# Kernel optimization log

Measured on AMD Instinct MI355X. Metric: run time of the kernel, lower is better.

## Reference

```python
import jax, jax.numpy as jnp
import numpy as np

K_NEIGHBORS = 3  # init kwarg k_neighbors


def setup_inputs() -> dict:
    key = jax.random.key(0)
    k1, k2 = jax.random.split(key)
    q = jax.random.normal(k1, (75, 640, 21, 21), dtype=jnp.float32)
    S = jax.random.normal(k2, (5, 640, 21, 21), dtype=jnp.float32)
    return {"q": q, "S": S, "qAV_num": 1, "SAV_num": 1, "shot_num": 1}


def reference(q, S, qAV_num, SAV_num, shot_num):
    B, C = q.shape[0], q.shape[1]
    # [B, HW, C], L2-normalize each local descriptor over channels
    qd = q.reshape(B, C, -1).transpose(0, 2, 1)
    qd = qd / jnp.linalg.norm(qd, axis=2, keepdims=True)

    N = S.shape[0]
    sd = S.reshape(N, C, -1).transpose(0, 2, 1)  # [N, HW, C]
    sd = sd / jnp.linalg.norm(sd, axis=2, keepdims=True)
    HW = sd.shape[1]
    M = SAV_num * shot_num * HW
    # group support images into classes: [ncls, C, M]
    sup = sd.reshape(-1, M, C).transpose(0, 2, 1)
    ncls = sup.shape[0]

    # cosine similarity: [B, ncls, HW, M]
    ip = jnp.einsum('bqc,ncm->bnqm', qd, sup)
    # split AV groups: [B//qAV, qAV, ncls, HW, M]
    ip = ip.reshape(B // qAV_num, qAV_num, ncls, HW, M)
    # top-k along the query-descriptor (HW) axis (torch dim=-2)
    topk = jax.lax.top_k(jnp.swapaxes(ip, -1, -2), K_NEIGHBORS)[0]  # [..., M, k]
    img2class = topk.sum(axis=(-1, -2))  # [B', qAV, ncls]
    # geometric mean over the AV axis (dim=1)
    sim = jnp.exp(jnp.mean(jnp.log(img2class), axis=1))  # [B', ncls]
    return sim
```

## Files before the change

### kernel.cpp

```cpp
#include <hip/hip_runtime.h>
#include <hip/hip_bf16.h>


#define B_IMGS 75
#define N_CLS  5
#define C_DIM  640
#define HW     441
#define HWP    448
#define NKT    20
#define NRB    28
#define CHUNK  512

typedef __attribute__((ext_vector_type(8))) short  short8;
typedef __attribute__((ext_vector_type(4))) float  float4v;

__device__ __forceinline__ void ins3(float& t0, float& t1, float& t2, float v) {
    float m  = fminf(t0, v);
    t0 = fmaxf(t0, v);
    float m2 = fminf(t1, m);
    t1 = fmaxf(t1, m);
    t2 = fmaxf(t2, m2);
}

__device__ __forceinline__ void glds16(const __hip_bfloat16* g, __hip_bfloat16* l) {
    __builtin_amdgcn_global_load_lds(
        (const __attribute__((address_space(1))) unsigned int*)g,
        (__attribute__((address_space(3))) unsigned int*)l, 16, 0, 0);
}

__global__ __launch_bounds__(256)
void prep_kernel(const float* __restrict__ q, const float* __restrict__ S,
                 __hip_bfloat16* __restrict__ qn2, __hip_bfloat16* __restrict__ sn2) {
    __shared__ __hip_bfloat16 tile[C_DIM][65];
    __shared__ float part[4][64];
    __shared__ float inv[64];

    int bid = blockIdx.x;
    int img = bid / 7;
    int h0  = bid % 7;
    const float* src; __hip_bfloat16* dst;
    if (img < B_IMGS) {
        src = q + (size_t)img * C_DIM * HW;
        dst = qn2 + (size_t)img * NRB * NKT * CHUNK;
    } else {
        src = S + (size_t)(img - B_IMGS) * C_DIM * HW;
        dst = sn2 + (size_t)(img - B_IMGS) * NRB * NKT * CHUNK;
    }
    int t  = threadIdx.x;
    int hl = t & 63;
    int p  = t >> 6;
    int hw = h0 * 64 + hl;
    bool ok = hw < HW;
    int hwc = ok ? hw : (HW - 1);

    float ss = 0.f;
#pragma unroll 16
    for (int c = p * 160; c < (p + 1) * 160; ++c) {
        float v = src[(size_t)c * HW + hwc];
        ss += v * v;
    }
    part[p][hl] = ss;
    __syncthreads();
    if (t < 64) {
        float tot = part[0][t] + part[1][t] + part[2][t] + part[3][t];
        bool okr = (h0 * 64 + t) < HW;
        inv[t] = okr ? rsqrtf(tot) : 0.f;
    }
    __syncthreads();

    float iv = inv[hl];
#pragma unroll 8
    for (int c = p * 160; c < (p + 1) * 160; ++c) {
        float v = src[(size_t)c * HW + hwc] * iv;
        tile[c][hl] = __float2bfloat16(v);
    }
    __syncthreads();

    int rl  = t >> 2;
    int k8  = (t & 3) * 8;
    int rb  = h0 * 4 + (rl >> 4);
    int r16 = rl & 15;
    for (int kt = 0; kt < NKT; ++kt) {
        short8 v;
#pragma unroll
        for (int j = 0; j < 8; ++j) {
            __hip_bfloat16 h = tile[kt * 32 + k8 + j][rl];
            v[j] = *(short*)&h;
        }
        *(short8*)(dst + ((size_t)rb * NKT + kt) * CHUNK + r16 * 32 + k8) = v;
    }
}

__global__ __launch_bounds__(256, 2)
void gemm_top3_kernel(const __hip_bfloat16* __restrict__ qn2,
                      const __hip_bfloat16* __restrict__ sn2,
                      float* __restrict__ out) {
    __shared__ __hip_bfloat16 sbuf[64 * CHUNK];
    __shared__ float mrg[4][64][3];

    int id  = blockIdx.x;
    int xcd = id & 7;
    int j8  = id >> 3;
    int b   = (j8 / 35) * 8 + xcd;
    if (b >= B_IMGS) return;
    int inner = j8 % 35;
    int n  = inner / 7;
    int mt = inner % 7;

    int tid  = threadIdx.x;
    int w    = tid >> 6;
    int lane = tid & 63;
    int c16  = lane & 15;
    int quad = lane >> 4;
    int frag = c16 * 32 + quad * 8;

    const __hip_bfloat16* qA = qn2 + (size_t)b * NRB * NKT * CHUNK;
    const __hip_bfloat16* qB = sn2 + ((size_t)n * NRB + mt * 4) * NKT * CHUNK;

    float4v acc[7][4];
#pragma unroll
    for (int r = 0; r < 7; ++r)
#pragma unroll
        for (int j = 0; j < 4; ++j)
            acc[r][j] = (float4v){0.f, 0.f, 0.f, 0.f};

    for (int s = 0; s < 10; ++s) {
        __syncthreads();
#pragma unroll
        for (int i = 0; i < 16; ++i) {
            int cid = w * 16 + i;
            const __hip_bfloat16* g;
            if (cid < 56) {
                int rb = cid >> 1;
                g = qA + ((size_t)rb * NKT + 2 * s + (cid & 1)) * CHUNK;
            } else {
                int jb = (cid - 56) >> 1;
                g = qB + ((size_t)jb * NKT + 2 * s + (cid & 1)) * CHUNK;
            }
            glds16(g + lane * 8, sbuf + cid * CHUNK + lane * 8);
        }
        __syncthreads();

#pragma unroll
        for (int kk = 0; kk < 2; ++kk) {
            short8 a[7], bfr[4];
#pragma unroll
            for (int r = 0; r < 7; ++r)
                a[r] = *(const short8*)(sbuf + ((r * 4 + w) * 2 + kk) * CHUNK + frag);
#pragma unroll
            for (int j = 0; j < 4; ++j)
                bfr[j] = *(const short8*)(sbuf + (56 + j * 2 + kk) * CHUNK + frag);
#pragma unroll
            for (int r = 0; r < 7; ++r)
#pragma unroll
                for (int j = 0; j < 4; ++j)
                    acc[r][j] = __builtin_amdgcn_mfma_f32_16x16x32_bf16(
                        a[r], bfr[j], acc[r][j], 0, 0, 0);
        }
    }

    float T0[4], T1[4], T2[4];
#pragma unroll
    for (int j = 0; j < 4; ++j) { T0[j] = -1e30f; T1[j] = -1e30f; T2[j] = -1e30f; }
#pragma unroll
    for (int r = 0; r < 7; ++r)
#pragma unroll
        for (int j = 0; j < 4; ++j)
#pragma unroll
            for (int g = 0; g < 4; ++g) {
                int row = r * 64 + w * 16 + quad * 4 + g;
                float v = (row < HW) ? acc[r][j][g] : -1e30f;
                ins3(T0[j], T1[j], T2[j], v);
            }

#pragma unroll
    for (int j = 0; j < 4; ++j) {
#pragma unroll
        for (int d = 16; d <= 32; d <<= 1) {
            float o0 = __shfl_xor(T0[j], d, 64);
            float o1 = __shfl_xor(T1[j], d, 64);
            float o2 = __shfl_xor(T2[j], d, 64);
            ins3(T0[j], T1[j], T2[j], o0);
            ins3(T0[j], T1[j], T2[j], o1);
            ins3(T0[j], T1[j], T2[j], o2);
        }
    }

    if (quad == 0) {
#pragma unroll
        for (int j = 0; j < 4; ++j) {
            mrg[w][j * 16 + c16][0] = T0[j];
            mrg[w][j * 16 + c16][1] = T1[j];
            mrg[w][j * 16 + c16][2] = T2[j];
        }
    }
    __syncthreads();
    if (tid < 64) {
        int col = tid;
        float t0 = mrg[0][col][0], t1 = mrg[0][col][1], t2 = mrg[0][col][2];
#pragma unroll
        for (int ww = 1; ww < 4; ++ww) {
            ins3(t0, t1, t2, mrg[ww][col][0]);
            ins3(t0, t1, t2, mrg[ww][col][1]);
            ins3(t0, t1, t2, mrg[ww][col][2]);
        }
        float s = (mt * 64 + col < HW) ? (t0 + t1 + t2) : 0.f;
#pragma unroll
        for (int d = 32; d >= 1; d >>= 1) s += __shfl_xor(s, d, 64);
        if (tid == 0) atomicAdd(&out[b * N_CLS + n], s);
    }
}

extern "C" void kernel_launch(void* const* d_in, const int* in_sizes, int n_in,
                              void* d_out, int out_size, void* d_ws, size_t ws_size,
                              hipStream_t stream) {
    const float* q = (const float*)d_in[0];
    const float* S = (const float*)d_in[1];
    float* out = (float*)d_out;

    char* ws = (char*)d_ws;
    size_t off = 0;
    __hip_bfloat16* qn2 = (__hip_bfloat16*)(ws + off);
    off += (size_t)B_IMGS * NRB * NKT * CHUNK * 2;  off = (off + 255) & ~(size_t)255;
    __hip_bfloat16* sn2 = (__hip_bfloat16*)(ws + off);

    hipMemsetAsync(d_out, 0, (size_t)out_size * sizeof(float), stream);

    prep_kernel<<<dim3(80 * 7), dim3(256), 0, stream>>>(q, S, qn2, sn2);
    gemm_top3_kernel<<<dim3(8 * 350), dim3(256), 0, stream>>>(qn2, sn2, out);
}
```

Before: 291.3 us.

## Defer L2 normalization to GEMM epilogue and split prep across channel slices

The prep kernel no longer normalizes before the bf16 conversion. It splits each image into 5 channel slices, reads the input once, writes raw bf16 tiles, and accumulates squared norms with atomics. A small finish kernel turns those sums into inverse norms. The GEMM then scales query rows by the inverse norm before the top-3 selection, and scales the per-column sums by the support inverse norm. The GEMM is also restructured to 448 threads (7 waves) with a 32-chunk LDS buffer and one k-tile per step, cutting registers and LDS to raise occupancy. In exchange it adds two launches, a memset and atomics, and it rounds unnormalized values to bf16.

```diff
diff --git a/kernel.cpp b/kernel.cpp
--- a/kernel.cpp
+++ b/kernel.cpp
@@ -22,6 +22,11 @@
     t2 = fmaxf(t2, m2);
 }
 
+__device__ __forceinline__ short bf16bits(float x) {
+    __hip_bfloat16 h = __float2bfloat16(x);
+    return *(short*)&h;
+}
+
 __device__ __forceinline__ void glds16(const __hip_bfloat16* g, __hip_bfloat16* l) {
     __builtin_amdgcn_global_load_lds(
         (const __attribute__((address_space(1))) unsigned int*)g,
@@ -30,14 +35,16 @@
 
 __global__ __launch_bounds__(256)
 void prep_kernel(const float* __restrict__ q, const float* __restrict__ S,
-                 __hip_bfloat16* __restrict__ qn2, __hip_bfloat16* __restrict__ sn2) {
-    __shared__ __hip_bfloat16 tile[C_DIM][65];
+                 __hip_bfloat16* __restrict__ qn2, __hip_bfloat16* __restrict__ sn2,
+                 float* __restrict__ normAll) {
+    __shared__ float tile[128][65];
     __shared__ float part[4][64];
-    __shared__ float inv[64];
 
     int bid = blockIdx.x;
-    int img = bid / 7;
-    int h0  = bid % 7;
+    int img = bid / 35;
+    int rem = bid % 35;
+    int h0  = rem / 5;
+    int cs  = rem % 5;
     const float* src; __hip_bfloat16* dst;
     if (img < B_IMGS) {
         src = q + (size_t)img * C_DIM * HW;
@@ -51,52 +58,52 @@
     int p  = t >> 6;
     int hw = h0 * 64 + hl;
     bool ok = hw < HW;
-    int hwc = ok ? hw : (HW - 1);
 
     float ss = 0.f;
-#pragma unroll 16
-    for (int c = p * 160; c < (p + 1) * 160; ++c) {
-        float v = src[(size_t)c * HW + hwc];
+#pragma unroll
+    for (int i = 0; i < 32; ++i) {
+        int cl = p * 32 + i;
+        float v = ok ? src[(size_t)(cs * 128 + cl) * HW + hw] : 0.f;
+        tile[cl][hl] = v;
         ss += v * v;
     }
     part[p][hl] = ss;
     __syncthreads();
-    if (t < 64) {
+    if (t < 64 && (h0 * 64 + t) < HW) {
         float tot = part[0][t] + part[1][t] + part[2][t] + part[3][t];
-        bool okr = (h0 * 64 + t) < HW;
-        inv[t] = okr ? rsqrtf(tot) : 0.f;
-    }
-    __syncthreads();
-
-    float iv = inv[hl];
-#pragma unroll 8
-    for (int c = p * 160; c < (p + 1) * 160; ++c) {
-        float v = src[(size_t)c * HW + hwc] * iv;
-        tile[c][hl] = __float2bfloat16(v);
-    }
-    __syncthreads();
-
-    int rl  = t >> 2;
-    int k8  = (t & 3) * 8;
-    int rb  = h0 * 4 + (rl >> 4);
-    int r16 = rl & 15;
-    for (int kt = 0; kt < NKT; ++kt) {
+        atomicAdd(normAll + img * HWP + h0 * 64 + t, tot);
+    }
+
+    int rbl   = t >> 6;
+    int l     = t & 63;
+    int seg   = l >> 4;
+    int row16 = l & 15;
+#pragma unroll
+    for (int ktl = 0; ktl < 4; ++ktl) {
         short8 v;
 #pragma unroll
-        for (int j = 0; j < 8; ++j) {
-            __hip_bfloat16 h = tile[kt * 32 + k8 + j][rl];
-            v[j] = *(short*)&h;
-        }
-        *(short8*)(dst + ((size_t)rb * NKT + kt) * CHUNK + r16 * 32 + k8) = v;
-    }
-}
-
-__global__ __launch_bounds__(256, 2)
+        for (int j = 0; j < 8; ++j)
+            v[j] = bf16bits(tile[ktl * 32 + seg * 8 + j][rbl * 16 + row16]);
+        size_t coff = ((size_t)(h0 * 4 + rbl) * NKT + cs * 4 + ktl) * CHUNK;
+        *(short8*)(dst + coff + l * 8) = v;
+    }
+}
+
+__global__ void finish_kernel(float* __restrict__ normAll) {
+    int i = blockIdx.x * blockDim.x + threadIdx.x;
+    if (i < (B_IMGS + N_CLS) * HWP) {
+        float s = normAll[i];
+        normAll[i] = (s > 0.f) ? rsqrtf(s) : 0.f;
+    }
+}
+
+__global__ __launch_bounds__(448, 4)
 void gemm_top3_kernel(const __hip_bfloat16* __restrict__ qn2,
                       const __hip_bfloat16* __restrict__ sn2,
+                      const float* __restrict__ normAll,
                       float* __restrict__ out) {
-    __shared__ __hip_bfloat16 sbuf[64 * CHUNK];
-    __shared__ float mrg[4][64][3];
+    __shared__ __hip_bfloat16 sbuf[32 * CHUNK];
+    __shared__ float mrg[7][64][3];
 
     int id  = blockIdx.x;
     int xcd = id & 7;
@@ -109,69 +116,66 @@
 
     int tid  = threadIdx.x;
     int w    = tid >> 6;
-    int lane = tid & 63;
-    int c16  = lane & 15;
-    int quad = lane >> 4;
-    int frag = c16 * 32 + quad * 8;
+    int l    = tid & 63;
+    int c16  = l & 15;
+    int quad = l >> 4;
 
     const __hip_bfloat16* qA = qn2 + (size_t)b * NRB * NKT * CHUNK;
     const __hip_bfloat16* qB = sn2 + ((size_t)n * NRB + mt * 4) * NKT * CHUNK;
 
-    float4v acc[7][4];
-#pragma unroll
-    for (int r = 0; r < 7; ++r)
+    float4v acc[4][4];
+#pragma unroll
+    for (int r = 0; r < 4; ++r)
 #pragma unroll
         for (int j = 0; j < 4; ++j)
             acc[r][j] = (float4v){0.f, 0.f, 0.f, 0.f};
 
-    for (int s = 0; s < 10; ++s) {
+    for (int s = 0; s < NKT; ++s) {
         __syncthreads();
 #pragma unroll
-        for (int i = 0; i < 16; ++i) {
-            int cid = w * 16 + i;
-            const __hip_bfloat16* g;
-            if (cid < 56) {
-                int rb = cid >> 1;
-                g = qA + ((size_t)rb * NKT + 2 * s + (cid & 1)) * CHUNK;
-            } else {
-                int jb = (cid - 56) >> 1;
-                g = qB + ((size_t)jb * NKT + 2 * s + (cid & 1)) * CHUNK;
+        for (int i = 0; i < 5; ++i) {
+            int c = i * 7 + w;
+            if (c < 32) {
+                const __hip_bfloat16* g = (c < 28)
+                    ? qA + ((size_t)c * NKT + s) * CHUNK
+                    : qB + ((size_t)(c - 28) * NKT + s) * CHUNK;
+                glds16(g + l * 8, sbuf + c * CHUNK + l * 8);
             }
-            glds16(g + lane * 8, sbuf + cid * CHUNK + lane * 8);
         }
         __syncthreads();
 
-#pragma unroll
-        for (int kk = 0; kk < 2; ++kk) {
-            short8 a[7], bfr[4];
-#pragma unroll
-            for (int r = 0; r < 7; ++r)
-                a[r] = *(const short8*)(sbuf + ((r * 4 + w) * 2 + kk) * CHUNK + frag);
+        short8 a[4], bf[4];
+#pragma unroll
+        for (int r = 0; r < 4; ++r)
+            a[r] = *(const short8*)(sbuf + (w * 4 + r) * CHUNK + l * 8);
+#pragma unroll
+        for (int j = 0; j < 4; ++j)
+            bf[j] = *(const short8*)(sbuf + (28 + j) * CHUNK + l * 8);
+#pragma unroll
+        for (int r = 0; r < 4; ++r)
 #pragma unroll
             for (int j = 0; j < 4; ++j)
-                bfr[j] = *(const short8*)(sbuf + (56 + j * 2 + kk) * CHUNK + frag);
-#pragma unroll
-            for (int r = 0; r < 7; ++r)
-#pragma unroll
-                for (int j = 0; j < 4; ++j)
-                    acc[r][j] = __builtin_amdgcn_mfma_f32_16x16x32_bf16(
-                        a[r], bfr[j], acc[r][j], 0, 0, 0);
-        }
-    }
-
+                acc[r][j] = __builtin_amdgcn_mfma_f32_16x16x32_bf16(
+                    a[r], bf[j], acc[r][j], 0, 0, 0);
+    }
+
+    const float* invq = normAll + (size_t)b * HWP;
     float T0[4], T1[4], T2[4];
 #pragma unroll
     for (int j = 0; j < 4; ++j) { T0[j] = -1e30f; T1[j] = -1e30f; T2[j] = -1e30f; }
 #pragma unroll
-    for (int r = 0; r < 7; ++r)
-#pragma unroll
-        for (int j = 0; j < 4; ++j)
-#pragma unroll
-            for (int g = 0; g < 4; ++g) {
-                int row = r * 64 + w * 16 + quad * 4 + g;
-                float v = (row < HW) ? acc[r][j][g] : -1e30f;
+    for (int r = 0; r < 4; ++r)
+#pragma unroll
+        for (int g = 0; g < 4; ++g) {
+            int row = w * 64 + r * 16 + quad * 4 + g;
+            float iv = invq[row];
+            bool valid = row < HW;
+#pragma unroll
+            for (int j = 0; j < 4; ++j) {
+                float v = valid ? acc[r][j][g] * iv : -1e30f;
                 ins3(T0[j], T1[j], T2[j], v);
             }
+        }
 
 #pragma unroll
     for (int j = 0; j < 4; ++j) {
@@ -199,12 +203,13 @@
         int col = tid;
         float t0 = mrg[0][col][0], t1 = mrg[0][col][1], t2 = mrg[0][col][2];
 #pragma unroll
-        for (int ww = 1; ww < 4; ++ww) {
+        for (int ww = 1; ww < 7; ++ww) {
             ins3(t0, t1, t2, mrg[ww][col][0]);
             ins3(t0, t1, t2, mrg[ww][col][1]);
             ins3(t0, t1, t2, mrg[ww][col][2]);
         }
-        float s = (mt * 64 + col < HW) ? (t0 + t1 + t2) : 0.f;
+        float isv = normAll[(size_t)(B_IMGS + n) * HWP + mt * 64 + col];
+        float s = (mt * 64 + col < HW) ? (t0 + t1 + t2) * isv : 0.f;
 #pragma unroll
         for (int d = 32; d >= 1; d >>= 1) s += __shfl_xor(s, d, 64);
         if (tid == 0) atomicAdd(&out[b * N_CLS + n], s);
@@ -223,9 +228,13 @@
     __hip_bfloat16* qn2 = (__hip_bfloat16*)(ws + off);
     off += (size_t)B_IMGS * NRB * NKT * CHUNK * 2;  off = (off + 255) & ~(size_t)255;
     __hip_bfloat16* sn2 = (__hip_bfloat16*)(ws + off);
+    off += (size_t)N_CLS * NRB * NKT * CHUNK * 2;   off = (off + 255) & ~(size_t)255;
+    float* normAll = (float*)(ws + off);
 
     hipMemsetAsync(d_out, 0, (size_t)out_size * sizeof(float), stream);
-
-    prep_kernel<<<dim3(80 * 7), dim3(256), 0, stream>>>(q, S, qn2, sn2);
-    gemm_top3_kernel<<<dim3(8 * 350), dim3(256), 0, stream>>>(qn2, sn2, out);
-}
+    hipMemsetAsync(normAll, 0, (size_t)(B_IMGS + N_CLS) * HWP * sizeof(float), stream);
+
+    prep_kernel<<<dim3(80 * 35), dim3(256), 0, stream>>>(q, S, qn2, sn2, normAll);
+    finish_kernel<<<dim3(((B_IMGS + N_CLS) * HWP + 255) / 256), dim3(256), 0, stream>>>(normAll);
+    gemm_top3_kernel<<<dim3(8 * 350), dim3(448), 0, stream>>>(qn2, sn2, normAll, out);
+}
```

After: 317.6 us. 1.09x slower.

## Defer L2 normalization to epilogue and read inputs once in prep kernel

Applied to the files above, without the earlier changes.

The prep kernel now splits each image by channel slices, reads each input element once, writes unnormalized bf16 packed tiles and partial squared norms. The GEMM kernel reduces the partial norms into inverse norms and applies them to the accumulator during top-3 selection. This is valid because the scaling is positive, and for the support side it can be applied after selection. It also preloads the first K stage before the norm reduction and restructures the loop so the load/sync sits at the end of each iteration. The input read traffic in prep is halved, at the cost of extra norm reads and a different bf16 rounding of unnormalized values.

```diff
diff --git a/kernel.cpp b/kernel.cpp
--- a/kernel.cpp
+++ b/kernel.cpp
@@ -4,6 +4,7 @@
 
 #define B_IMGS 75
 #define N_CLS  5
+#define N_IMGS 80
 #define C_DIM  640
 #define HW     441
 #define HWP    448
@@ -30,73 +31,62 @@
 
 __global__ __launch_bounds__(256)
 void prep_kernel(const float* __restrict__ q, const float* __restrict__ S,
-                 __hip_bfloat16* __restrict__ qn2, __hip_bfloat16* __restrict__ sn2) {
-    __shared__ __hip_bfloat16 tile[C_DIM][65];
-    __shared__ float part[4][64];
-    __shared__ float inv[64];
-
+                 __hip_bfloat16* __restrict__ pk, float* __restrict__ normPart) {
+    __shared__ __hip_bfloat16 tile[64][449];
     int bid = blockIdx.x;
-    int img = bid / 7;
-    int h0  = bid % 7;
-    const float* src; __hip_bfloat16* dst;
-    if (img < B_IMGS) {
-        src = q + (size_t)img * C_DIM * HW;
-        dst = qn2 + (size_t)img * NRB * NKT * CHUNK;
-    } else {
-        src = S + (size_t)(img - B_IMGS) * C_DIM * HW;
-        dst = sn2 + (size_t)(img - B_IMGS) * NRB * NKT * CHUNK;
-    }
-    int t  = threadIdx.x;
-    int hl = t & 63;
-    int p  = t >> 6;
-    int hw = h0 * 64 + hl;
-    bool ok = hw < HW;
-    int hwc = ok ? hw : (HW - 1);
-
-    float ss = 0.f;
-#pragma unroll 16
-    for (int c = p * 160; c < (p + 1) * 160; ++c) {
-        float v = src[(size_t)c * HW + hwc];
-        ss += v * v;
-    }
-    part[p][hl] = ss;
+    int img = bid / 10;
+    int cs  = bid % 10;
+    const float* src = (img < B_IMGS)
+        ? q + (size_t)img * C_DIM * HW
+        : S + (size_t)(img - B_IMGS) * C_DIM * HW;
+    __hip_bfloat16* dst = pk + (size_t)img * NRB * NKT * CHUNK;
+    const float* base = src + (size_t)cs * 64 * HW;
+
+    int t = threadIdx.x;
+    bool t2ok = (t < HW - 256);
+    float ss0 = 0.f, ss1 = 0.f;
+#pragma unroll 4
+    for (int cl = 0; cl < 64; ++cl) {
+        float v0 = base[cl * HW + t];
+        float v1 = t2ok ? base[cl * HW + 256 + t] : 0.f;
+        ss0 += v0 * v0;
+        ss1 += v1 * v1;
+        tile[cl][t] = __float2bfloat16(v0);
+        if (t < HWP - 256) tile[cl][256 + t] = __float2bfloat16(v1);
+    }
+    normPart[((size_t)cs * N_IMGS + img) * HWP + t] = ss0;
+    if (t < HWP - 256)
+        normPart[((size_t)cs * N_IMGS + img) * HWP + 256 + t] = ss1;
     __syncthreads();
-    if (t < 64) {
-        float tot = part[0][t] + part[1][t] + part[2][t] + part[3][t];
-        bool okr = (h0 * 64 + t) < HW;
-        inv[t] = okr ? rsqrtf(tot) : 0.f;
-    }
-    __syncthreads();
-
-    float iv = inv[hl];
-#pragma unroll 8
-    for (int c = p * 160; c < (p + 1) * 160; ++c) {
-        float v = src[(size_t)c * HW + hwc] * iv;
-        tile[c][hl] = __float2bfloat16(v);
-    }
-    __syncthreads();
-
-    int rl  = t >> 2;
-    int k8  = (t & 3) * 8;
-    int rb  = h0 * 4 + (rl >> 4);
-    int r16 = rl & 15;
-    for (int kt = 0; kt < NKT; ++kt) {
-        short8 v;
-#pragma unroll
-        for (int j = 0; j < 8; ++j) {
-            __hip_bfloat16 h = tile[kt * 32 + k8 + j][rl];
-            v[j] = *(short*)&h;
-        }
-        *(short8*)(dst + ((size_t)rb * NKT + kt) * CHUNK + r16 * 32 + k8) = v;
+
+    int l     = t & 63;
+    int wg    = t >> 6;
+    int row16 = l & 15;
+    int quad  = l >> 4;
+#pragma unroll
+    for (int i = 0; i < 7; ++i) {
+        int rb = i * 4 + wg;
+#pragma unroll
+        for (int kk = 0; kk < 2; ++kk) {
+            short8 v;
+#pragma unroll
+            for (int j = 0; j < 8; ++j) {
+                __hip_bfloat16 h = tile[kk * 32 + quad * 8 + j][rb * 16 + row16];
+                v[j] = *(short*)&h;
+            }
+            *(short8*)(dst + ((size_t)rb * NKT + cs * 2 + kk) * CHUNK + l * 8) = v;
+        }
     }
 }
 
 __global__ __launch_bounds__(256, 2)
-void gemm_top3_kernel(const __hip_bfloat16* __restrict__ qn2,
-                      const __hip_bfloat16* __restrict__ sn2,
+void gemm_top3_kernel(const __hip_bfloat16* __restrict__ pk,
+                      const float* __restrict__ normPart,
                       float* __restrict__ out) {
     __shared__ __hip_bfloat16 sbuf[64 * CHUNK];
     __shared__ float mrg[4][64][3];
+    __shared__ float sInvQ[HWP];
+    __shared__ float sInvS[64];
 
     int id  = blockIdx.x;
     int xcd = id & 7;
@@ -109,13 +99,38 @@
 
     int tid  = threadIdx.x;
     int w    = tid >> 6;
-    int lane = tid & 63;
-    int c16  = lane & 15;
-    int quad = lane >> 4;
-    int frag = c16 * 32 + quad * 8;
-
-    const __hip_bfloat16* qA = qn2 + (size_t)b * NRB * NKT * CHUNK;
-    const __hip_bfloat16* qB = sn2 + ((size_t)n * NRB + mt * 4) * NKT * CHUNK;
+    int l    = tid & 63;
+    int c16  = l & 15;
+    int quad = l >> 4;
+
+    const __hip_bfloat16* qA = pk + (size_t)b * NRB * NKT * CHUNK;
+    const __hip_bfloat16* qB = pk + ((size_t)(B_IMGS + n) * NRB + mt * 4) * NKT * CHUNK;
+
+#pragma unroll
+    for (int i = 0; i < 16; ++i) {
+        int cid = w * 16 + i;
+        const __hip_bfloat16* g = (cid < 56)
+            ? qA + ((size_t)(cid >> 1) * NKT + (cid & 1)) * CHUNK
+            : qB + ((size_t)((cid - 56) >> 1) * NKT + (cid & 1)) * CHUNK;
+        glds16(g + l * 8, sbuf + cid * CHUNK + l * 8);
+    }
+
+    {
+        float s0 = 0.f, s1 = 0.f, s2 = 0.f;
+#pragma unroll
+        for (int cs = 0; cs < 10; ++cs) {
+            const float* npq = normPart + ((size_t)cs * N_IMGS + b) * HWP;
+            s0 += npq[tid];
+            if (tid < HWP - 256) s1 += npq[256 + tid];
+            if (tid < 64)
+                s2 += normPart[((size_t)cs * N_IMGS + B_IMGS + n) * HWP + mt * 64 + tid];
+        }
+        sInvQ[tid] = (tid < HW) ? rsqrtf(s0) : 0.f;
+        if (tid < HWP - 256)
+            sInvQ[256 + tid] = ((256 + tid) < HW) ? rsqrtf(s1) : 0.f;
+        if (tid < 64)
+            sInvS[tid] = ((mt * 64 + tid) < HW) ? rsqrtf(s2) : 0.f;
+    }
 
     float4v acc[7][4];
 #pragma unroll
@@ -124,38 +139,36 @@
         for (int j = 0; j < 4; ++j)
             acc[r][j] = (float4v){0.f, 0.f, 0.f, 0.f};
 
+    __syncthreads();
+
     for (int s = 0; s < 10; ++s) {
-        __syncthreads();
-#pragma unroll
-        for (int i = 0; i < 16; ++i) {
-            int cid = w * 16 + i;
-            const __hip_bfloat16* g;
-            if (cid < 56) {
-                int rb = cid >> 1;
-                g = qA + ((size_t)rb * NKT + 2 * s + (cid & 1)) * CHUNK;
-            } else {
-                int jb = (cid - 56) >> 1;
-                g = qB + ((size_t)jb * NKT + 2 * s + (cid & 1)) * CHUNK;
-            }
-            glds16(g + lane * 8, sbuf + cid * CHUNK + lane * 8);
-        }
-        __syncthreads();
-
 #pragma unroll
         for (int kk = 0; kk < 2; ++kk) {
-            short8 a[7], bfr[4];
+            short8 a[7], bf[4];
 #pragma unroll
             for (int r = 0; r < 7; ++r)
-                a[r] = *(const short8*)(sbuf + ((r * 4 + w) * 2 + kk) * CHUNK + frag);
+                a[r] = *(const short8*)(sbuf + ((r * 4 + w) * 2 + kk) * CHUNK + l * 8);
 #pragma unroll
             for (int j = 0; j < 4; ++j)
-                bfr[j] = *(const short8*)(sbuf + (56 + j * 2 + kk) * CHUNK + frag);
+                bf[j] = *(const short8*)(sbuf + (56 + j * 2 + kk) * CHUNK + l * 8);
 #pragma unroll
             for (int r = 0; r < 7; ++r)
 #pragma unroll
                 for (int j = 0; j < 4; ++j)
                     acc[r][j] = __builtin_amdgcn_mfma_f32_16x16x32_bf16(
-                        a[r], bfr[j], acc[r][j], 0, 0, 0);
+                        a[r], bf[j], acc[r][j], 0, 0, 0);
+        }
+        if (s + 1 < 10) {
+            __syncthreads();
+#pragma unroll
+            for (int i = 0; i < 16; ++i) {
+                int cid = w * 16 + i;
+                const __hip_bfloat16* g = (cid < 56)
+                    ? qA + ((size_t)(cid >> 1) * NKT + 2 * (s + 1) + (cid & 1)) * CHUNK
+                    : qB + ((size_t)((cid - 56) >> 1) * NKT + 2 * (s + 1) + (cid & 1)) * CHUNK;
+                glds16(g + l * 8, sbuf + cid * CHUNK + l * 8);
+            }
+            __syncthreads();
         }
     }
 
@@ -165,13 +178,16 @@
 #pragma unroll
     for (int r = 0; r < 7; ++r)
 #pragma unroll
-        for (int j = 0; j < 4; ++j)
-#pragma unroll
-            for (int g = 0; g < 4; ++g) {
-                int row = r * 64 + w * 16 + quad * 4 + g;
-                float v = (row < HW) ? acc[r][j][g] : -1e30f;
+        for (int g = 0; g < 4; ++g) {
+            int row = r * 64 + w * 16 + quad * 4 + g;
+            float iv = sInvQ[row];
+            bool valid = row < HW;
+#pragma unroll
+            for (int j = 0; j < 4; ++j) {
+                float v = valid ? acc[r][j][g] * iv : -1e30f;
                 ins3(T0[j], T1[j], T2[j], v);
             }
+        }
 
 #pragma unroll
     for (int j = 0; j < 4; ++j) {
@@ -204,7 +220,8 @@
             ins3(t0, t1, t2, mrg[ww][col][1]);
             ins3(t0, t1, t2, mrg[ww][col][2]);
         }
-        float s = (mt * 64 + col < HW) ? (t0 + t1 + t2) : 0.f;
+        float isv = sInvS[col];
+        float s = (mt * 64 + col < HW) ? (t0 + t1 + t2) * isv : 0.f;
 #pragma unroll
         for (int d = 32; d >= 1; d >>= 1) s += __shfl_xor(s, d, 64);
         if (tid == 0) atomicAdd(&out[b * N_CLS + n], s);
@@ -220,12 +237,12 @@
 
     char* ws = (char*)d_ws;
     size_t off = 0;
-    __hip_bfloat16* qn2 = (__hip_bfloat16*)(ws + off);
-    off += (size_t)B_IMGS * NRB * NKT * CHUNK * 2;  off = (off + 255) & ~(size_t)255;
-    __hip_bfloat16* sn2 = (__hip_bfloat16*)(ws + off);
+    __hip_bfloat16* pk = (__hip_bfloat16*)(ws + off);
+    off += (size_t)N_IMGS * NRB * NKT * CHUNK * 2;  off = (off + 255) & ~(size_t)255;
+    float* normPart = (float*)(ws + off);
 
     hipMemsetAsync(d_out, 0, (size_t)out_size * sizeof(float), stream);
 
-    prep_kernel<<<dim3(80 * 7), dim3(256), 0, stream>>>(q, S, qn2, sn2);
-    gemm_top3_kernel<<<dim3(8 * 350), dim3(256), 0, stream>>>(qn2, sn2, out);
-}
+    prep_kernel<<<dim3(N_IMGS * 10), dim3(256), 0, stream>>>(q, S, pk, normPart);
+    gemm_top3_kernel<<<dim3(8 * 350), dim3(256), 0, stream>>>(pk, normPart, out);
+}
```

Result: slower. 347.0 us (+19.1%).
